# Performance work log

Hardware: AMD Instinct MI355X
Metric: run time of the kernel (lower is better)

The kernel has to match this reference:

```python
import jax, jax.numpy as jnp
import numpy as np

T = 2048; H = 1024; NH = 16; NKV = 4; HD = 64
E = 32; TOPK = 4; NG = 4; TG = 2; IM = 384; ISH = 384
ROT = HD // 2          # partial_rotary_factor = 0.5
EPS = 1e-5; RSF = 1.0; THETA = 10000.0


def setup_inputs() -> dict:
    ks = jax.random.split(jax.random.key(0), 12)
    g = lambda k, sh, sc=0.02: jax.random.normal(k, sh, jnp.float32) * sc
    return {
        "hidden_states": g(ks[0], (T, H), 1.0),
        "residual": g(ks[1], (T, H), 1.0),
        "in_ln_w": jnp.ones((H,), jnp.float32),
        "post_ln_w": jnp.ones((H,), jnp.float32),
        "q_norm_w": jnp.ones((HD,), jnp.float32),
        "k_norm_w": jnp.ones((HD,), jnp.float32),
        "Wqkv": g(ks[2], (H, (NH + 2 * NKV) * HD)),
        "Wo": g(ks[3], (NH * HD, H)),
        "Wg": g(ks[4], (H, E)),
        "gate_bias": g(ks[5], (E,), 0.1),
        "Wgu": g(ks[6], (E, H, 2 * IM)),
        "Wd": g(ks[7], (E, IM, H)),
        "Wgu_sh": g(ks[8], (H, 2 * ISH)),
        "Wd_sh": g(ks[9], (ISH, H)),
        "positions": jnp.arange(T, dtype=jnp.int32),
    }


def _rms(x, w):
    return x * jax.lax.rsqrt(jnp.mean(x * x, -1, keepdims=True) + EPS) * w


def _rope(x, pos):
    # neox-style rotary on the first ROT dims of each head; x: [T, nheads, HD]
    half = ROT // 2
    inv = THETA ** (-(jnp.arange(half, dtype=jnp.float32) * 2.0 / ROT))
    ang = pos.astype(jnp.float32)[:, None] * inv          # [T, half]
    c = jnp.cos(ang)[:, None, :]
    s = jnp.sin(ang)[:, None, :]
    x1, x2, rest = x[..., :half], x[..., half:ROT], x[..., ROT:]
    return jnp.concatenate([x1 * c - x2 * s, x1 * s + x2 * c, rest], -1)


def _layer(pos, hidden, residual, in_ln_w, post_ln_w, q_norm_w, k_norm_w,
           Wqkv, Wo, Wg, gate_bias, Wgu, Wd, Wgu_sh, Wd_sh):
    # fused add-RMSNorm (vllm RMSNorm(x, residual))
    residual = hidden + residual
    hidden = _rms(residual, in_ln_w)

    # self-attention (GQA, per-head qk-norm, partial rotary, causal)
    qkv = hidden @ Wqkv
    q = qkv[:, :NH * HD].reshape(T, NH, HD)
    k = qkv[:, NH * HD:(NH + NKV) * HD].reshape(T, NKV, HD)
    v = qkv[:, (NH + NKV) * HD:].reshape(T, NKV, HD)
    q = _rms(q, q_norm_w)
    k = _rms(k, k_norm_w)
    q = _rope(q, pos)
    k = _rope(k, pos)
    rep = NH // NKV
    k = jnp.repeat(k, rep, axis=1)
    v = jnp.repeat(v, rep, axis=1)
    scores = jnp.einsum('thd,shd->hts', q, k) * (HD ** -0.5)
    causal = pos[:, None] >= pos[None, :]
    scores = jnp.where(causal[None], scores, -jnp.inf)
    attn = jax.nn.softmax(scores, axis=-1)
    o = jnp.einsum('hts,shd->thd', attn, v).reshape(T, NH * HD)
    hidden = o @ Wo

    # post-attention fused add-RMSNorm
    residual = hidden + residual
    hidden = _rms(residual, post_ln_w)

    # --- Glm4MoE: grouped sigmoid top-k router with e_score_correction_bias ---
    logits = hidden.astype(jnp.float32) @ Wg            # gate runs in fp32
    scr = jax.nn.sigmoid(logits)                        # [T, E]
    sfc = scr + gate_bias                               # scores_for_choice
    # group score = sum of top-2 biased scores within each group
    gs = jnp.sum(jax.lax.top_k(sfc.reshape(T, NG, E // NG), 2)[0], -1)  # [T, NG]
    _, gidx = jax.lax.top_k(gs, TG)
    gmask = jnp.zeros((T, NG), jnp.float32).at[jnp.arange(T)[:, None], gidx].set(1.0)
    emask = jnp.repeat(gmask, E // NG, axis=1)          # [T, E]
    _, ids = jax.lax.top_k(jnp.where(emask > 0, sfc, -jnp.inf), TOPK)
    w = jnp.take_along_axis(scr, ids, axis=1)           # weights from unbiased scores
    w = w / jnp.sum(w, -1, keepdims=True)               # renormalize (norm_topk_prob)
    wdense = jnp.zeros((T, E), jnp.float32).at[jnp.arange(T)[:, None], ids].set(w)

    # routed experts: dense-over-experts reference for the grouped GEMM dispatch
    gu = jnp.einsum('th,ehi->tei', hidden, Wgu)         # [T, E, 2*IM]
    act = jax.nn.silu(gu[..., :IM]) * gu[..., IM:]      # SiluAndMul
    routed = jnp.einsum('te,tei,eih->th', wdense, act, Wd)

    # shared expert MLP
    gus = hidden @ Wgu_sh
    shared = (jax.nn.silu(gus[:, :ISH]) * gus[:, ISH:]) @ Wd_sh

    hidden = routed * RSF + shared
    return hidden, residual


def reference(hidden_states, residual, in_ln_w, post_ln_w, q_norm_w, k_norm_w,
              Wqkv, Wo, Wg, gate_bias, Wgu, Wd, Wgu_sh, Wd_sh, positions):
    return _layer(positions, hidden_states, residual, in_ln_w, post_ln_w,
                  q_norm_w, k_norm_w, Wqkv, Wo, Wg, gate_bias, Wgu, Wd,
                  Wgu_sh, Wd_sh)
```

## Files before the change

### kernel.cpp

```cpp
#include <hip/hip_runtime.h>
#include <math.h>

#define TT 2048
#define HH 1024
#define NHEADS 16
#define NKVH 4
#define HDIM 64
#define NEXP 32
#define TOPK_ 4
#define NGRP 4
#define IMID 384
#define ISHARED 384
#define QKV_W (24*64)
#define EPS_ 1e-5f
#define MAXSB 288
#define NSPLITS 80

typedef __attribute__((ext_vector_type(8))) short short8;
typedef __attribute__((ext_vector_type(4))) float f32x4;

__device__ __forceinline__ ushort f2bf(float x) {
  union { float f; unsigned u; } v; v.f = x;
  unsigned r = v.u + 0x7fffu + ((v.u >> 16) & 1u);
  return (ushort)(r >> 16);
}
__device__ __forceinline__ float bf2f(ushort u) {
  union { unsigned i; float f; } v; v.i = (unsigned)u << 16; return v.f;
}

__device__ __forceinline__ void gload16(const void* g, void* l) {
  __builtin_amdgcn_global_load_lds(
      (const __attribute__((address_space(1))) unsigned int*)g,
      (__attribute__((address_space(3))) unsigned int*)l, 16, 0, 0);
}

__device__ __forceinline__ short8 read_a_frag64(const ushort* As, int lg, int row) {
  return *(const short8*)(As + ((lg * 64 + (row ^ lg)) * 8));
}
__device__ __forceinline__ short8 read_b_frag(const ushort* Bs, int lg, int col) {
  int boff = (col * 16) ^ (((col >> 3) & 7) << 4);
  return *(const short8*)((const char*)Bs + lg * 1024 + boff);
}

__device__ __forceinline__ void stage_B_tile(const float* __restrict__ B, int ldb,
                                             int k0, int col0, ushort* Bs, int tid) {
  int a = tid >> 4;
  int cG = tid & 15;
  int k = 2 * a;
  const float* p0 = B + (size_t)(k0 + k) * ldb + col0 + cG * 4;
  const float* p1 = p0 + ldb;
  float4 r0 = *(const float4*)p0;
  float4 r1 = *(const float4*)p1;
  int gg = (k & 15) >> 2;
  int slot = (k & 3) + ((k >> 4) << 2);
  float v0[4] = {r0.x, r0.y, r0.z, r0.w};
  float v1[4] = {r1.x, r1.y, r1.z, r1.w};
  char* plane = (char*)Bs + gg * 1024;
  #pragma unroll
  for (int j = 0; j < 4; ++j) {
    int c = cG * 4 + j;
    unsigned pk = (unsigned)f2bf(v0[j]) | ((unsigned)f2bf(v1[j]) << 16);
    int boff = ((c * 16) ^ (((c >> 3) & 7) << 4)) + slot * 2;
    *(unsigned*)(plane + boff) = pk;
  }
}

__global__ __launch_bounds__(256) void pack_B_kernel(
    const float* __restrict__ src, ushort* __restrict__ dst, int N) {
  __shared__ ushort tileB[2048];
  int tid = threadIdx.x;
  stage_B_tile(src, N, blockIdx.y * 32, blockIdx.x * 64, tileB, tid);
  __syncthreads();
  size_t toff = ((size_t)blockIdx.y * gridDim.x + blockIdx.x) * 2048;
  *(short8*)(dst + toff + tid * 8) = *(const short8*)(tileB + tid * 8);
}

__global__ __launch_bounds__(256) void gemm64_bb(
    const ushort* __restrict__ Ab, const ushort* __restrict__ Bpk,
    float* __restrict__ C, int M, int N, int K) {
  __shared__ ushort As[4][2048];
  __shared__ ushort Bs[4][2048];
  int tid = threadIdx.x;
  int row0 = blockIdx.y * 64, col0 = blockIdx.x * 64;
  int ntn = N >> 6;
  int wid = tid >> 6, lane = tid & 63;
  int lg = lane >> 4, lr = lane & 15;
  int wrow = (wid >> 1) * 32, wcol = (wid & 1) * 32;
  const ushort* asrc = Ab + (size_t)(row0 + (lane ^ wid)) * K + wid * 8;
  const ushort* bsrc = Bpk + (size_t)blockIdx.x * 2048 + wid * 512 + lane * 8;
  const int NT = K >> 5;
  f32x4 acc[2][2] = {};

  auto issue = [&](int tt) {
    int b = tt & 3;
    gload16(asrc + tt * 32, &As[b][wid * 512]);
    gload16(bsrc + (size_t)tt * ntn * 2048, &Bs[b][wid * 512]);
  };
  issue(0); issue(1); issue(2);
  for (int t = 0; t < NT; ++t) {
    int ahead = NT - 1 - t;
    if (ahead >= 2)      asm volatile("s_waitcnt vmcnt(4)" ::: "memory");
    else if (ahead == 1) asm volatile("s_waitcnt vmcnt(2)" ::: "memory");
    else                 asm volatile("s_waitcnt vmcnt(0)" ::: "memory");
    __builtin_amdgcn_s_barrier();
    if (t + 3 < NT) issue(t + 3);
    int cb = t & 3;
    short8 af0 = read_a_frag64(&As[cb][0], lg, wrow + lr);
    short8 af1 = read_a_frag64(&As[cb][0], lg, wrow + 16 + lr);
    #pragma unroll
    for (int nn = 0; nn < 2; ++nn) {
      short8 bf_ = read_b_frag(&Bs[cb][0], lg, wcol + nn * 16 + lr);
      acc[0][nn] = __builtin_amdgcn_mfma_f32_16x16x32_bf16(af0, bf_, acc[0][nn], 0, 0, 0);
      acc[1][nn] = __builtin_amdgcn_mfma_f32_16x16x32_bf16(af1, bf_, acc[1][nn], 0, 0, 0);
    }
  }
  #pragma unroll
  for (int mm = 0; mm < 2; ++mm)
    #pragma unroll
    for (int nn = 0; nn < 2; ++nn) {
      int row = row0 + wrow + mm * 16 + lg * 4;
      int col = col0 + wcol + nn * 16 + lr;
      #pragma unroll
      for (int i = 0; i < 4; ++i)
        C[(size_t)(row + i) * N + col] = acc[mm][nn][i];
    }
}

__global__ __launch_bounds__(256) void moe_up_pk(
    const ushort* __restrict__ hln2b, const ushort* __restrict__ Wpk,
    const int* __restrict__ perm, const int* __restrict__ offs,
    const int* __restrict__ counts, const int* __restrict__ sb_e,
    const int* __restrict__ sb_base, const int* __restrict__ nsb,
    ushort* __restrict__ actb) {
  int b = blockIdx.x;
  int sb = ((b & 7) * 36) + (b >> 3);
  if (sb >= *nsb) return;
  int e = sb_e[sb];
  int base = sb_base[sb];
  int start = offs[e];
  int nt = min(32, counts[e] - base);
  int tid = threadIdx.x;
  int wid = tid >> 6, lane = tid & 63;
  int lg = lane >> 4, lr = lane & 15;
  int bz = blockIdx.y * 2 + (wid >> 1);
  int wcol = (wid & 1) * 32;
  int tok0 = perm[start + base + min(lr, nt - 1)] >> 2;
  int tok1 = perm[start + base + min(16 + lr, nt - 1)] >> 2;
  const ushort* a0p = hln2b + (size_t)tok0 * HH + lg * 8;
  const ushort* a1p = hln2b + (size_t)tok1 * HH + lg * 8;
  int c0 = wcol + lr, c1 = wcol + 16 + lr;
  int sw0 = (c0 * 16) ^ (((c0 >> 3) & 7) << 4);
  int sw1 = (c1 * 16) ^ (((c1 >> 3) & 7) << 4);
  const char* gbase = (const char*)Wpk + ((size_t)(e * 32) * 12 + bz) * 4096 + lg * 1024;
  const char* ubase = gbase + (size_t)6 * 4096;
  const size_t bstep = (size_t)12 * 4096;
  f32x4 accg[2][2] = {}, accu[2][2] = {};
  short8 a0c = *(const short8*)(a0p);
  short8 a1c = *(const short8*)(a1p);
  short8 g0c = *(const short8*)(gbase + sw0);
  short8 g1c = *(const short8*)(gbase + sw1);
  short8 u0c = *(const short8*)(ubase + sw0);
  short8 u1c = *(const short8*)(ubase + sw1);
  #pragma unroll 4
  for (int t = 0; t < 31; ++t) {
    const char* gb = gbase + (size_t)(t + 1) * bstep;
    const char* ub = ubase + (size_t)(t + 1) * bstep;
    short8 a0n = *(const short8*)(a0p + (t + 1) * 32);
    short8 a1n = *(const short8*)(a1p + (t + 1) * 32);
    short8 g0n = *(const short8*)(gb + sw0);
    short8 g1n = *(const short8*)(gb + sw1);
    short8 u0n = *(const short8*)(ub + sw0);
    short8 u1n = *(const short8*)(ub + sw1);
    accg[0][0] = __builtin_amdgcn_mfma_f32_16x16x32_bf16(a0c, g0c, accg[0][0], 0, 0, 0);
    accg[0][1] = __builtin_amdgcn_mfma_f32_16x16x32_bf16(a0c, g1c, accg[0][1], 0, 0, 0);
    accg[1][0] = __builtin_amdgcn_mfma_f32_16x16x32_bf16(a1c, g0c, accg[1][0], 0, 0, 0);
    accg[1][1] = __builtin_amdgcn_mfma_f32_16x16x32_bf16(a1c, g1c, accg[1][1], 0, 0, 0);
    accu[0][0] = __builtin_amdgcn_mfma_f32_16x16x32_bf16(a0c, u0c, accu[0][0], 0, 0, 0);
    accu[0][1] = __builtin_amdgcn_mfma_f32_16x16x32_bf16(a0c, u1c, accu[0][1], 0, 0, 0);
    accu[1][0] = __builtin_amdgcn_mfma_f32_16x16x32_bf16(a1c, u0c, accu[1][0], 0, 0, 0);
    accu[1][1] = __builtin_amdgcn_mfma_f32_16x16x32_bf16(a1c, u1c, accu[1][1], 0, 0, 0);
    a0c = a0n; a1c = a1n; g0c = g0n; g1c = g1n; u0c = u0n; u1c = u1n;
  }
  accg[0][0] = __builtin_amdgcn_mfma_f32_16x16x32_bf16(a0c, g0c, accg[0][0], 0, 0, 0);
  accg[0][1] = __builtin_amdgcn_mfma_f32_16x16x32_bf16(a0c, g1c, accg[0][1], 0, 0, 0);
  accg[1][0] = __builtin_amdgcn_mfma_f32_16x16x32_bf16(a1c, g0c, accg[1][0], 0, 0, 0);
  accg[1][1] = __builtin_amdgcn_mfma_f32_16x16x32_bf16(a1c, g1c, accg[1][1], 0, 0, 0);
  accu[0][0] = __builtin_amdgcn_mfma_f32_16x16x32_bf16(a0c, u0c, accu[0][0], 0, 0, 0);
  accu[0][1] = __builtin_amdgcn_mfma_f32_16x16x32_bf16(a0c, u1c, accu[0][1], 0, 0, 0);
  accu[1][0] = __builtin_amdgcn_mfma_f32_16x16x32_bf16(a1c, u0c, accu[1][0], 0, 0, 0);
  accu[1][1] = __builtin_amdgcn_mfma_f32_16x16x32_bf16(a1c, u1c, accu[1][1], 0, 0, 0);
  #pragma unroll
  for (int mm = 0; mm < 2; ++mm)
    #pragma unroll
    for (int nn = 0; nn < 2; ++nn) {
      int pcol = bz * 64 + wcol + ((lr >> 2) << 3) + (nn << 2) + (lr & 3);
      #pragma unroll
      for (int i = 0; i < 4; ++i) {
        int rr = mm * 16 + lg * 4 + i;
        if (rr < nt) {
          float gv = accg[mm][nn][i], uv = accu[mm][nn][i];
          float av = gv / (1.f + expf(-gv)) * uv;
          actb[(size_t)(start + base + rr) * IMID + pcol] = f2bf(av);
        }
      }
    }
}

__global__ __launch_bounds__(256) void moe_down_pk(
    const ushort* __restrict__ actb, const ushort* __restrict__ Wpk,
    const int* __restrict__ offs, const int* __restrict__ counts,
    const int* __restrict__ sb_e, const int* __restrict__ sb_base,
    const int* __restrict__ nsb, ushort* __restrict__ partialb) {
  int b = blockIdx.x;
  int sb = ((b & 7) * 36) + (b >> 3);
  if (sb >= *nsb) return;
  int e = sb_e[sb];
  int base = sb_base[sb];
  int start = offs[e];
  int nt = min(32, counts[e] - base);
  int tid = threadIdx.x;
  int wid = tid >> 6, lane = tid & 63;
  int lg = lane >> 4, lr = lane & 15;
  int nct = blockIdx.y * 2 + (wid >> 1);
  int wcol = (wid & 1) * 32;
  const ushort* a0p = actb + (size_t)(start + base + min(lr, nt - 1)) * IMID + lg * 8;
  const ushort* a1p = actb + (size_t)(start + base + min(16 + lr, nt - 1)) * IMID + lg * 8;
  int c0 = wcol + lr, c1 = wcol + 16 + lr;
  int sw0 = (c0 * 16) ^ (((c0 >> 3) & 7) << 4);
  int sw1 = (c1 * 16) ^ (((c1 >> 3) & 7) << 4);
  const char* bbase = (const char*)Wpk + ((size_t)(e * 12) * 16 + nct) * 4096 + lg * 1024;
  const size_t bstep = (size_t)16 * 4096;
  f32x4 acc[2][2] = {};
  short8 a0c = *(const short8*)(a0p);
  short8 a1c = *(const short8*)(a1p);
  short8 b0c = *(const short8*)(bbase + sw0);
  short8 b1c = *(const short8*)(bbase + sw1);
  #pragma unroll 4
  for (int t = 0; t < 11; ++t) {
    const char* bb = bbase + (size_t)(t + 1) * bstep;
    short8 a0n = *(const short8*)(a0p + (t + 1) * 32);
    short8 a1n = *(const short8*)(a1p + (t + 1) * 32);
    short8 b0n = *(const short8*)(bb + sw0);
    short8 b1n = *(const short8*)(bb + sw1);
    acc[0][0] = __builtin_amdgcn_mfma_f32_16x16x32_bf16(a0c, b0c, acc[0][0], 0, 0, 0);
    acc[0][1] = __builtin_amdgcn_mfma_f32_16x16x32_bf16(a0c, b1c, acc[0][1], 0, 0, 0);
    acc[1][0] = __builtin_amdgcn_mfma_f32_16x16x32_bf16(a1c, b0c, acc[1][0], 0, 0, 0);
    acc[1][1] = __builtin_amdgcn_mfma_f32_16x16x32_bf16(a1c, b1c, acc[1][1], 0, 0, 0);
    a0c = a0n; a1c = a1n; b0c = b0n; b1c = b1n;
  }
  acc[0][0] = __builtin_amdgcn_mfma_f32_16x16x32_bf16(a0c, b0c, acc[0][0], 0, 0, 0);
  acc[0][1] = __builtin_amdgcn_mfma_f32_16x16x32_bf16(a0c, b1c, acc[0][1], 0, 0, 0);
  acc[1][0] = __builtin_amdgcn_mfma_f32_16x16x32_bf16(a1c, b0c, acc[1][0], 0, 0, 0);
  acc[1][1] = __builtin_amdgcn_mfma_f32_16x16x32_bf16(a1c, b1c, acc[1][1], 0, 0, 0);
  #pragma unroll
  for (int mm = 0; mm < 2; ++mm)
    #pragma unroll
    for (int nn = 0; nn < 2; ++nn)
      #pragma unroll
      for (int i = 0; i < 4; ++i) {
        int rr = mm * 16 + lg * 4 + i;
        if (rr < nt)
          partialb[(size_t)(start + base + rr) * HH + nct * 64 + wcol + nn * 16 + lr] = f2bf(acc[mm][nn][i]);
      }
}

__global__ __launch_bounds__(256) void add_rms_kernel(
    const float* __restrict__ a, const float* __restrict__ b,
    const float* __restrict__ w, float* __restrict__ sum_out,
    float* __restrict__ ln_out, ushort* __restrict__ lnb) {
  int t = blockIdx.x, tid = threadIdx.x;
  float4 x = reinterpret_cast<const float4*>(a + (size_t)t*HH)[tid];
  float4 y = reinterpret_cast<const float4*>(b + (size_t)t*HH)[tid];
  x.x += y.x; x.y += y.y; x.z += y.z; x.w += y.w;
  float ss = x.x*x.x + x.y*x.y + x.z*x.z + x.w*x.w;
  #pragma unroll
  for (int off = 1; off < 64; off <<= 1) ss += __shfl_xor(ss, off);
  __shared__ float wsum[4];
  int wid = tid >> 6, lane = tid & 63;
  if (lane == 0) wsum[wid] = ss;
  __syncthreads();
  float tot = wsum[0] + wsum[1] + wsum[2] + wsum[3];
  float r = rsqrtf(tot * (1.0f/HH) + EPS_);
  reinterpret_cast<float4*>(sum_out + (size_t)t*HH)[tid] = x;
  float4 wl = reinterpret_cast<const float4*>(w)[tid];
  float4 o = make_float4(x.x*r*wl.x, x.y*r*wl.y, x.z*r*wl.z, x.w*r*wl.w);
  reinterpret_cast<float4*>(ln_out + (size_t)t*HH)[tid] = o;
  ushort4 ub;
  ub.x = f2bf(o.x); ub.y = f2bf(o.y); ub.z = f2bf(o.z); ub.w = f2bf(o.w);
  int dst = ((tid >> 3) << 5) + ((tid & 3) << 3) + (((tid >> 2) & 1) << 2);
  *(ushort4*)(lnb + (size_t)t * HH + dst) = ub;
}

__global__ __launch_bounds__(256) void qk_norm_rope_kernel(
    float* __restrict__ qkv, const float* __restrict__ qw,
    const float* __restrict__ kw, const int* __restrict__ pos) {
  int t = blockIdx.x;
  int hh = blockIdx.y * 4 + (threadIdx.x >> 6);
  int lane = threadIdx.x & 63;
  float* p = qkv + (size_t)t * QKV_W + hh * HDIM;
  float x = p[lane];
  float ss = x * x;
  #pragma unroll
  for (int off = 1; off < 64; off <<= 1) ss += __shfl_xor(ss, off);
  float r = rsqrtf(ss * (1.0f/HDIM) + EPS_);
  float wv = (hh < NHEADS ? qw : kw)[lane];
  float xn = x * r * wv;
  float partner = __shfl_xor(xn, 16);
  float out = xn;
  if (lane < 32) {
    int i = lane & 15;
    float inv = powf(10000.0f, -(float)i / 16.0f);
    float ang = (float)pos[t] * inv;
    float cv = cosf(ang), sv = sinf(ang);
    out = (lane < 16) ? (xn * cv - partner * sv) : (partner * sv + xn * cv);
  }
  p[lane] = out;
}

__global__ __launch_bounds__(256) void pack_KV_kernel(
    const float* __restrict__ qkv, ushort* __restrict__ Kpk,
    ushort* __restrict__ Vpk) {
  __shared__ ushort kimg[2048];
  __shared__ ushort vimg[2048];
  int tid = threadIdx.x;
  int kt = blockIdx.x, kvh = blockIdx.y;
  {
    int c = tid >> 7, t2 = tid & 127;
    int g = t2 & 3, r = t2 >> 2;
    const float* kp = qkv + (size_t)(kt*32 + r) * QKV_W + NHEADS*HDIM + kvh*HDIM + 32*c + 4*g;
    float4 h0 = *(const float4*)kp;
    float4 h1 = *(const float4*)(kp + 16);
    short8 v;
    v[0]=(short)f2bf(h0.x); v[1]=(short)f2bf(h0.y); v[2]=(short)f2bf(h0.z); v[3]=(short)f2bf(h0.w);
    v[4]=(short)f2bf(h1.x); v[5]=(short)f2bf(h1.y); v[6]=(short)f2bf(h1.z); v[7]=(short)f2bf(h1.w);
    *(short8*)(kimg + c*1024 + (g*32 + (r^g))*8) = v;
  }
  stage_B_tile(qkv + (size_t)(NHEADS+NKVH)*HDIM + (size_t)kvh*HDIM, QKV_W, kt*32, 0, vimg, tid);
  __syncthreads();
  size_t toff = ((size_t)(kvh * (TT/32) + kt)) * 2048;
  *(short8*)(Kpk + toff + tid * 8) = *(const short8*)(kimg + tid * 8);
  *(short8*)(Vpk + toff + tid * 8) = *(const short8*)(vimg + tid * 8);
}

__global__ __launch_bounds__(256) void attn_v3_kernel(
    const float* __restrict__ qkv, const ushort* __restrict__ Kpk,
    const ushort* __restrict__ Vpk, ushort* __restrict__ ob,
    float* __restrict__ po, float* __restrict__ pl) {
  __shared__ ushort Ks[3][2048];
  __shared__ ushort Vs[3][2048];
  int tid = threadIdx.x;
  int wid = tid >> 6, lane = tid & 63;
  int lg = lane >> 4, lr = lane & 15;
  int h = blockIdx.y;
  int f = blockIdx.x;
  int g = 0;
  while (f >= 4 * (g + 1) * (g + 2)) ++g;
  int r_ = f - 4 * g * (g + 1);
  int ns = g + 1;
  int qb = 8 * g + r_ / ns;
  int s = r_ % ns;
  int tiles_total = 2 * qb + 2;
  int per = (tiles_total + ns - 1) / ns;
  int lo = s * per;
  int nloc = min(per, tiles_total - lo);
  int kvh = h >> 2;
  int q0 = qb * 64 + wid * 16;
  int qg = q0 + lr;
  const float SCL = 0.125f * 1.44269504f;
  const float FM = 16.0f;

  const float* qrow = qkv + (size_t)qg * QKV_W + h * HDIM;
  short8 qfr[2];
  #pragma unroll
  for (int c = 0; c < 2; ++c) {
    float4 a = *(const float4*)(qrow + 32*c + 4*lg);
    float4 b = *(const float4*)(qrow + 32*c + 4*lg + 16);
    short8 v;
    v[0]=(short)f2bf(a.x*SCL); v[1]=(short)f2bf(a.y*SCL); v[2]=(short)f2bf(a.z*SCL); v[3]=(short)f2bf(a.w*SCL);
    v[4]=(short)f2bf(b.x*SCL); v[5]=(short)f2bf(b.y*SCL); v[6]=(short)f2bf(b.z*SCL); v[7]=(short)f2bf(b.w*SCL);
    qfr[c] = v;
  }

  const ushort* ksrc = Kpk + (size_t)(kvh * (TT/32) + lo) * 2048 + wid * 512 + lane * 8;
  const ushort* vsrc = Vpk + (size_t)(kvh * (TT/32) + lo) * 2048 + wid * 512 + lane * 8;

  f32x4 o_acc[4] = {};
  float l_st = 0.f;

  auto issue = [&](int tt) {
    int b = tt % 3;
    gload16(ksrc + (size_t)tt * 2048, &Ks[b][wid * 512]);
    gload16(vsrc + (size_t)tt * 2048, &Vs[b][wid * 512]);
  };
  issue(0);
  if (nloc > 1) issue(1);
  for (int tt = 0; tt < nloc; ++tt) {
    if (tt < nloc - 1) asm volatile("s_waitcnt vmcnt(2)" ::: "memory");
    else               asm volatile("s_waitcnt vmcnt(0)" ::: "memory");
    __builtin_amdgcn_s_barrier();
    if (tt + 2 < nloc) issue(tt + 2);
    int t = lo + tt;
    if (t * 32 > q0 + 15) continue;
    int cb = tt % 3;
    f32x4 st[2];
    #pragma unroll
    for (int n = 0; n < 2; ++n) {
      short8 kf0 = *(const short8*)(&Ks[cb][(lg*32 + ((16*n + lr) ^ lg)) * 8]);
      short8 kf1 = *(const short8*)(&Ks[cb][1024 + (lg*32 + ((16*n + lr) ^ lg)) * 8]);
      f32x4 z = {};
      z = __builtin_amdgcn_mfma_f32_16x16x32_bf16(kf0, qfr[0], z, 0, 0, 0);
      st[n] = __builtin_amdgcn_mfma_f32_16x16x32_bf16(kf1, qfr[1], z, 0, 0, 0);
    }
    float p[2][4];
    float psum = 0.f;
    if (t * 32 + 31 <= q0) {
      #pragma unroll
      for (int n = 0; n < 2; ++n)
        #pragma unroll
        for (int i = 0; i < 4; ++i) {
          float pv = exp2f(st[n][i] - FM);
          p[n][i] = pv; psum += pv;
        }
    } else {
      #pragma unroll
      for (int n = 0; n < 2; ++n)
        #pragma unroll
        for (int i = 0; i < 4; ++i) {
          int kvg = t*32 + 16*n + 4*lg + i;
          float pv = (kvg <= qg) ? exp2f(st[n][i] - FM) : 0.f;
          p[n][i] = pv; psum += pv;
        }
    }
    psum += __shfl_xor(psum, 16);
    psum += __shfl_xor(psum, 32);
    l_st += psum;
    union { unsigned u[4]; short8 s8; } pu;
    asm volatile("v_cvt_pk_bf16_f32 %0, %1, %2" : "=v"(pu.u[0]) : "v"(p[0][0]), "v"(p[0][1]));
    asm volatile("v_cvt_pk_bf16_f32 %0, %1, %2" : "=v"(pu.u[1]) : "v"(p[0][2]), "v"(p[0][3]));
    asm volatile("v_cvt_pk_bf16_f32 %0, %1, %2" : "=v"(pu.u[2]) : "v"(p[1][0]), "v"(p[1][1]));
    asm volatile("v_cvt_pk_bf16_f32 %0, %1, %2" : "=v"(pu.u[3]) : "v"(p[1][2]), "v"(p[1][3]));
    short8 pa = pu.s8;
    #pragma unroll
    for (int nd = 0; nd < 4; ++nd) {
      short8 vf = read_b_frag(&Vs[cb][0], lg, 16*nd + lr);
      o_acc[nd] = __builtin_amdgcn_mfma_f32_16x16x32_bf16(pa, vf, o_acc[nd], 0, 0, 0);
    }
  }

  if (ns == 1) {
    #pragma unroll
    for (int i = 0; i < 4; ++i) {
      float lrow = __shfl(l_st, 4*lg + i);
      float inv = 1.0f / lrow;
      int row = q0 + 4*lg + i;
      ushort* op = ob + (size_t)row * (NHEADS*HDIM) + h * HDIM;
      #pragma unroll
      for (int nd = 0; nd < 4; ++nd) {
        int pcol = ((nd >> 1) << 5) + ((lr >> 2) << 3) + ((nd & 1) << 2) + (lr & 3);
        op[pcol] = f2bf(o_acc[nd][i] * inv);
      }
    }
  } else {
    float* pob = po + ((size_t)f * NHEADS + h) * 4096;
    #pragma unroll
    for (int nd = 0; nd < 4; ++nd)
      #pragma unroll
      for (int i = 0; i < 4; ++i)
        pob[(wid * 16 + lg * 4 + i) * 64 + 16 * nd + lr] = o_acc[nd][i];
    if (lg == 0)
      pl[((size_t)f * NHEADS + h) * 64 + wid * 16 + lr] = l_st;
  }
}

__global__ __launch_bounds__(256) void attn_combine_kernel(
    const float* __restrict__ po, const float* __restrict__ pl,
    ushort* __restrict__ ob) {
  int h = blockIdx.x;
  int qb = 8 + blockIdx.y;
  int g = qb >> 3;
  int ns = g + 1;
  int f0 = 4 * g * (g + 1) + (qb - 8 * g) * ns;
  int tid = threadIdx.x;
  int r = tid >> 2, c = tid & 3;
  float acc[16] = {};
  float lsum = 0.f;
  for (int s = 0; s < ns; ++s) {
    size_t base = ((size_t)(f0 + s) * NHEADS + h) * 4096 + r * 64 + c * 16;
    #pragma unroll
    for (int j = 0; j < 4; ++j) {
      float4 v = *(const float4*)(po + base + j * 4);
      acc[j*4+0] += v.x; acc[j*4+1] += v.y; acc[j*4+2] += v.z; acc[j*4+3] += v.w;
    }
    lsum += pl[((size_t)(f0 + s) * NHEADS + h) * 64 + r];
  }
  float inv = 1.0f / lsum;
  int row = qb * 64 + r;
  ushort* op = ob + (size_t)row * (NHEADS*HDIM) + h * HDIM + (c >> 1) * 32 + (c & 1) * 4;
  #pragma unroll
  for (int a = 0; a < 4; ++a) {
    ushort4 u;
    u.x = f2bf(acc[a*4+0] * inv); u.y = f2bf(acc[a*4+1] * inv);
    u.z = f2bf(acc[a*4+2] * inv); u.w = f2bf(acc[a*4+3] * inv);
    *(ushort4*)(op + a * 8) = u;
  }
}

__global__ __launch_bounds__(256) void router_kernel(
    const float* __restrict__ hln, const float* __restrict__ Wg,
    const float* __restrict__ bias, int* __restrict__ sel_e,
    float* __restrict__ sel_w) {
  __shared__ float hid[4][HH];
  int tid = threadIdx.x, wid = tid >> 6, lane = tid & 63;
  int t = blockIdx.x * 4 + wid;
  const float4* src = (const float4*)(hln + (size_t)t * HH);
  float4* dst = (float4*)hid[wid];
  #pragma unroll
  for (int j = 0; j < 4; ++j) dst[j * 64 + lane] = src[j * 64 + lane];
  int e = lane & 31, half = lane >> 5;
  const float* wp = Wg + (size_t)(half * 512) * NEXP + e;
  const float* hp = hid[wid] + half * 512;
  float p = 0.f;
  #pragma unroll 8
  for (int h = 0; h < 512; ++h) p += hp[h] * wp[(size_t)h * NEXP];
  p += __shfl_xor(p, 32);
  float sc = 1.0f / (1.0f + expf(-p));
  float sfc = sc + bias[e];
  float m1 = sfc, m2 = -1e30f;
  #pragma unroll
  for (int off = 1; off <= 4; off <<= 1) {
    float om1 = __shfl_xor(m1, off), om2 = __shfl_xor(m2, off);
    float hi_ = fmaxf(m1, om1);
    float lo_ = fmaxf(fminf(m1, om1), fmaxf(m2, om2));
    m1 = hi_; m2 = lo_;
  }
  float gs = m1 + m2;
  float gv[4] = {__shfl(gs, 0), __shfl(gs, 8), __shfl(gs, 16), __shfl(gs, 24)};
  int g1 = 0; float b1 = gv[0];
  #pragma unroll
  for (int g = 1; g < 4; ++g) if (gv[g] > b1) { b1 = gv[g]; g1 = g; }
  int g2 = -1; float b2 = -1e30f;
  #pragma unroll
  for (int g = 0; g < 4; ++g) if (g != g1 && gv[g] > b2) { b2 = gv[g]; g2 = g; }
  bool keep = ((e >> 3) == g1) || ((e >> 3) == g2);
  float cand = keep ? sfc : -1e30f;
  int ids[4]; float wv[4]; float wsum = 0.f;
  #pragma unroll
  for (int s = 0; s < 4; ++s) {
    float v = cand; int ix = e;
    #pragma unroll
    for (int off = 1; off < 64; off <<= 1) {
      float ov = __shfl_xor(v, off); int oix = __shfl_xor(ix, off);
      if (ov > v || (ov == v && oix < ix)) { v = ov; ix = oix; }
    }
    ids[s] = ix;
    if (e == ix) cand = -1e30f;
    float w = __shfl(sc, ix);
    wv[s] = w; wsum += w;
  }
  if (lane == 0) {
    #pragma unroll
    for (int s = 0; s < 4; ++s) {
      sel_e[t * 4 + s] = ids[s];
      sel_w[t * 4 + s] = wv[s] / wsum;
    }
  }
}

__global__ __launch_bounds__(256) void count_kernel(
    const int* __restrict__ sel_e, int* __restrict__ counts) {
  int e = blockIdx.x, tid = threadIdx.x;
  int c = 0;
  for (int i = tid; i < TT * TOPK_; i += 256) c += (sel_e[i] == e);
  #pragma unroll
  for (int off = 1; off < 64; off <<= 1) c += __shfl_xor(c, off);
  __shared__ int wsum[4];
  if ((tid & 63) == 0) wsum[tid >> 6] = c;
  __syncthreads();
  if (tid == 0) counts[e] = wsum[0] + wsum[1] + wsum[2] + wsum[3];
}

__global__ void scan_kernel(const int* __restrict__ counts,
                            int* __restrict__ offs, int* __restrict__ cursor,
                            int* __restrict__ sb_e, int* __restrict__ sb_base,
                            int* __restrict__ nsb) {
  if (threadIdx.x == 0) {
    int acc = 0, n = 0;
    for (int e = 0; e < NEXP; ++e) {
      offs[e] = acc; cursor[e] = acc;
      int c = counts[e];
      for (int b = 0; b < c; b += 32) { sb_e[n] = e; sb_base[n] = b; ++n; }
      acc += c;
    }
    *nsb = n;
  }
}

__global__ void scatter_kernel(const int* __restrict__ sel_e,
                               int* __restrict__ cursor, int* __restrict__ perm,
                               int* __restrict__ ipos) {
  int i = blockIdx.x * 256 + threadIdx.x;
  if (i < TT * TOPK_) {
    int e = sel_e[i];
    int pos = atomicAdd(&cursor[e], 1);
    perm[pos] = i;
    ipos[i] = pos;
  }
}

__global__ __launch_bounds__(256) void silu_shared_kernel(
    const float* __restrict__ gus, ushort* __restrict__ shsb) {
  int i = blockIdx.x * 256 + threadIdx.x;
  if (i < TT * (ISHARED/4)) {
    int t = i / (ISHARED/4), k = i % (ISHARED/4);
    const float* gp = gus + (size_t)t * (2*ISHARED) + k * 4;
    float4 g4 = *(const float4*)gp;
    float4 u4 = *(const float4*)(gp + ISHARED);
    ushort4 r;
    r.x = f2bf(g4.x / (1.f + expf(-g4.x)) * u4.x);
    r.y = f2bf(g4.y / (1.f + expf(-g4.y)) * u4.y);
    r.z = f2bf(g4.z / (1.f + expf(-g4.z)) * u4.z);
    r.w = f2bf(g4.w / (1.f + expf(-g4.w)) * u4.w);
    int pdst = ((k >> 3) << 5) + ((k & 3) << 3) + (((k >> 2) & 1) << 2);
    *(ushort4*)(shsb + (size_t)t * ISHARED + pdst) = r;
  }
}

__global__ __launch_bounds__(256) void final_combine_kernel(
    const ushort* __restrict__ partialb, const float* __restrict__ sel_w,
    const int* __restrict__ ipos, const float* __restrict__ shared_out,
    float* __restrict__ out_hidden) {
  int t = blockIdx.x, tid = threadIdx.x;
  float w0 = sel_w[t*4], w1 = sel_w[t*4+1], w2 = sel_w[t*4+2], w3 = sel_w[t*4+3];
  int p0 = ipos[t*4], p1 = ipos[t*4+1], p2 = ipos[t*4+2], p3 = ipos[t*4+3];
  ushort4 a0 = *(const ushort4*)(partialb + (size_t)p0*HH + tid*4);
  ushort4 a1 = *(const ushort4*)(partialb + (size_t)p1*HH + tid*4);
  ushort4 a2 = *(const ushort4*)(partialb + (size_t)p2*HH + tid*4);
  ushort4 a3 = *(const ushort4*)(partialb + (size_t)p3*HH + tid*4);
  float4 sh = reinterpret_cast<const float4*>(shared_out + (size_t)t*HH)[tid];
  float4 r;
  r.x = (w0*bf2f(a0.x) + w1*bf2f(a1.x) + w2*bf2f(a2.x) + w3*bf2f(a3.x)) + sh.x;
  r.y = (w0*bf2f(a0.y) + w1*bf2f(a1.y) + w2*bf2f(a2.y) + w3*bf2f(a3.y)) + sh.y;
  r.z = (w0*bf2f(a0.z) + w1*bf2f(a1.z) + w2*bf2f(a2.z) + w3*bf2f(a3.z)) + sh.z;
  r.w = (w0*bf2f(a0.w) + w1*bf2f(a1.w) + w2*bf2f(a2.w) + w3*bf2f(a3.w)) + sh.w;
  reinterpret_cast<float4*>(out_hidden + (size_t)t*HH)[tid] = r;
}

extern "C" void kernel_launch(void* const* d_in, const int* in_sizes, int n_in,
                              void* d_out, int out_size, void* d_ws, size_t ws_size,
                              hipStream_t stream) {
  const float* hidden   = (const float*)d_in[0];
  const float* residual = (const float*)d_in[1];
  const float* in_ln_w  = (const float*)d_in[2];
  const float* post_ln_w= (const float*)d_in[3];
  const float* q_norm_w = (const float*)d_in[4];
  const float* k_norm_w = (const float*)d_in[5];
  const float* Wqkv     = (const float*)d_in[6];
  const float* Wo       = (const float*)d_in[7];
  const float* Wg       = (const float*)d_in[8];
  const float* gate_bias= (const float*)d_in[9];
  const float* Wgu      = (const float*)d_in[10];
  const float* Wd       = (const float*)d_in[11];
  const float* Wgu_sh   = (const float*)d_in[12];
  const float* Wd_sh    = (const float*)d_in[13];
  const int*   positions= (const int*)d_in[14];
  float* out = (float*)d_out;

  float* f = (float*)d_ws;
  size_t off = 0;
  float* R_A   = f + off; off += (size_t)TT*HH;
  float* HLN   = f + off; off += (size_t)TT*HH;
  float* QKV   = f + off; off += (size_t)TT*QKV_W;
  float* OATT  = f + off; off += (size_t)TT*HH;
  float* HLN2  = f + off; off += (size_t)TT*HH;
  float* SELW  = f + off; off += (size_t)TT*TOPK_;
  float* PO    = f + off; off += (size_t)NSPLITS*NHEADS*4096;
  float* PL    = f + off; off += (size_t)NSPLITS*NHEADS*64;
  ushort* HLNB  = (ushort*)(f + off); off += (size_t)TT*HH/2;
  ushort* HLN2B = (ushort*)(f + off); off += (size_t)TT*HH/2;
  ushort* OATTB = (ushort*)(f + off); off += (size_t)TT*HH/2;
  ushort* SHSB  = (ushort*)(f + off); off += (size_t)TT*ISHARED/2;
  ushort* KPK   = (ushort*)(f + off); off += (size_t)NKVH*(TT/32)*2048/2;
  ushort* VPK   = (ushort*)(f + off); off += (size_t)NKVH*(TT/32)*2048/2;
  ushort* ACTB  = (ushort*)(f + off); off += (size_t)(TT*TOPK_ + 128)*IMID/2;
  ushort* PARTB = (ushort*)(f + off); off += (size_t)TT*TOPK_*HH/2;
  ushort* PK_QKV = (ushort*)(f + off); off += (size_t)HH*QKV_W/2;
  ushort* PK_WO  = (ushort*)(f + off); off += (size_t)HH*HH/2;
  ushort* PK_WGU = (ushort*)(f + off); off += (size_t)NEXP*HH*(2*IMID)/2;
  ushort* PK_WD  = (ushort*)(f + off); off += (size_t)NEXP*IMID*HH/2;
  ushort* PK_GUSH= (ushort*)(f + off); off += (size_t)HH*(2*ISHARED)/2;
  ushort* PK_DSH = (ushort*)(f + off); off += (size_t)ISHARED*HH/2;
  int* ibase   = (int*)(f + off);
  int* SELE    = ibase;
  int* PERM    = ibase + TT*TOPK_;
  int* IPOS    = ibase + 2*TT*TOPK_;
  int* COUNTS  = ibase + 3*TT*TOPK_;
  int* OFFS    = COUNTS + NEXP;
  int* CURSOR  = OFFS + NEXP;
  int* SB_E    = CURSOR + NEXP;
  int* SB_BASE = SB_E + MAXSB;
  int* NSB     = SB_BASE + MAXSB;

  pack_B_kernel<<<dim3(QKV_W/64, HH/32), 256, 0, stream>>>(Wqkv, PK_QKV, QKV_W);
  pack_B_kernel<<<dim3(HH/64, HH/32), 256, 0, stream>>>(Wo, PK_WO, HH);
  pack_B_kernel<<<dim3((2*IMID)/64, NEXP*HH/32), 256, 0, stream>>>(Wgu, PK_WGU, 2*IMID);
  pack_B_kernel<<<dim3(HH/64, NEXP*IMID/32), 256, 0, stream>>>(Wd, PK_WD, HH);
  pack_B_kernel<<<dim3((2*ISHARED)/64, HH/32), 256, 0, stream>>>(Wgu_sh, PK_GUSH, 2*ISHARED);
  pack_B_kernel<<<dim3(HH/64, ISHARED/32), 256, 0, stream>>>(Wd_sh, PK_DSH, HH);

  add_rms_kernel<<<TT, 256, 0, stream>>>(hidden, residual, in_ln_w, R_A, HLN, HLNB);
  gemm64_bb<<<dim3(QKV_W/64, TT/64), 256, 0, stream>>>(HLNB, PK_QKV, QKV, TT, QKV_W, HH);
  qk_norm_rope_kernel<<<dim3(TT, 5), 256, 0, stream>>>(QKV, q_norm_w, k_norm_w, positions);
  pack_KV_kernel<<<dim3(TT/32, NKVH), 256, 0, stream>>>(QKV, KPK, VPK);
  attn_v3_kernel<<<dim3(NSPLITS, NHEADS), 256, 0, stream>>>(QKV, KPK, VPK, OATTB, PO, PL);
  attn_combine_kernel<<<dim3(NHEADS, 24), 256, 0, stream>>>(PO, PL, OATTB);
  gemm64_bb<<<dim3(HH/64, TT/64), 256, 0, stream>>>(OATTB, PK_WO, HLN, TT, HH, HH);
  add_rms_kernel<<<TT, 256, 0, stream>>>(HLN, R_A, post_ln_w, out + (size_t)TT*HH, HLN2, HLN2B);
  router_kernel<<<TT/4, 256, 0, stream>>>(HLN2, Wg, gate_bias, SELE, SELW);
  count_kernel<<<NEXP, 256, 0, stream>>>(SELE, COUNTS);
  scan_kernel<<<1, 64, 0, stream>>>(COUNTS, OFFS, CURSOR, SB_E, SB_BASE, NSB);
  scatter_kernel<<<(TT*TOPK_ + 255)/256, 256, 0, stream>>>(SELE, CURSOR, PERM, IPOS);
  moe_up_pk<<<dim3(MAXSB, 3), 256, 0, stream>>>(HLN2B, PK_WGU, PERM, OFFS, COUNTS, SB_E, SB_BASE, NSB, ACTB);
  moe_down_pk<<<dim3(MAXSB, 8), 256, 0, stream>>>(ACTB, PK_WD, OFFS, COUNTS, SB_E, SB_BASE, NSB, PARTB);
  gemm64_bb<<<dim3((2*ISHARED)/64, TT/64), 256, 0, stream>>>(HLN2B, PK_GUSH, QKV, TT, 2*ISHARED, HH);
  silu_shared_kernel<<<(TT*(ISHARED/4) + 255)/256, 256, 0, stream>>>(QKV, SHSB);
  gemm64_bb<<<dim3(HH/64, TT/64), 256, 0, stream>>>(SHSB, PK_DSH, OATT, TT, HH, ISHARED);
  final_combine_kernel<<<TT, 256, 0, stream>>>(PARTB, SELW, IPOS, OATT, out);
}
```

Measured before the change: 361.6 us.

## Repartition MoE up-projection warps by row and batch weight packing tiles per block

```diff
diff --git a/kernel.cpp b/kernel.cpp
--- a/kernel.cpp
+++ b/kernel.cpp
@@ -65,14 +65,20 @@
   }
 }
 
-__global__ __launch_bounds__(256) void pack_B_kernel(
+__global__ __launch_bounds__(256) void pack_B4_kernel(
     const float* __restrict__ src, ushort* __restrict__ dst, int N) {
   __shared__ ushort tileB[2048];
   int tid = threadIdx.x;
-  stage_B_tile(src, N, blockIdx.y * 32, blockIdx.x * 64, tileB, tid);
-  __syncthreads();
-  size_t toff = ((size_t)blockIdx.y * gridDim.x + blockIdx.x) * 2048;
-  *(short8*)(dst + toff + tid * 8) = *(const short8*)(tileB + tid * 8);
+  int ntn = gridDim.x;
+  #pragma unroll
+  for (int kk = 0; kk < 4; ++kk) {
+    int kt = blockIdx.y * 4 + kk;
+    stage_B_tile(src, N, kt * 32, blockIdx.x * 64, tileB, tid);
+    __syncthreads();
+    size_t toff = ((size_t)kt * ntn + blockIdx.x) * 2048;
+    *(short8*)(dst + toff + tid * 8) = *(const short8*)(tileB + tid * 8);
+    __syncthreads();
+  }
 }
 
 __global__ __launch_bounds__(256) void gemm64_bb(
@@ -142,21 +148,21 @@
   int tid = threadIdx.x;
   int wid = tid >> 6, lane = tid & 63;
   int lg = lane >> 4, lr = lane & 15;
-  int bz = blockIdx.y * 2 + (wid >> 1);
+  int bz = blockIdx.y;
+  int rh = wid >> 1;
   int wcol = (wid & 1) * 32;
-  int tok0 = perm[start + base + min(lr, nt - 1)] >> 2;
-  int tok1 = perm[start + base + min(16 + lr, nt - 1)] >> 2;
-  const ushort* a0p = hln2b + (size_t)tok0 * HH + lg * 8;
-  const ushort* a1p = hln2b + (size_t)tok1 * HH + lg * 8;
+  int row = rh * 16 + lr;
+  int rowc = min(row, nt - 1);
+  int tok = perm[start + base + rowc] >> 2;
+  const ushort* ap = hln2b + (size_t)tok * HH + lg * 8;
   int c0 = wcol + lr, c1 = wcol + 16 + lr;
   int sw0 = (c0 * 16) ^ (((c0 >> 3) & 7) << 4);
   int sw1 = (c1 * 16) ^ (((c1 >> 3) & 7) << 4);
   const char* gbase = (const char*)Wpk + ((size_t)(e * 32) * 12 + bz) * 4096 + lg * 1024;
   const char* ubase = gbase + (size_t)6 * 4096;
   const size_t bstep = (size_t)12 * 4096;
-  f32x4 accg[2][2] = {}, accu[2][2] = {};
-  short8 a0c = *(const short8*)(a0p);
-  short8 a1c = *(const short8*)(a1p);
+  f32x4 ag0 = {}, ag1 = {}, au0 = {}, au1 = {};
+  short8 ac  = *(const short8*)ap;
   short8 g0c = *(const short8*)(gbase + sw0);
   short8 g1c = *(const short8*)(gbase + sw1);
   short8 u0c = *(const short8*)(ubase + sw0);
@@ -165,45 +171,35 @@
   for (int t = 0; t < 31; ++t) {
     const char* gb = gbase + (size_t)(t + 1) * bstep;
     const char* ub = ubase + (size_t)(t + 1) * bstep;
-    short8 a0n = *(const short8*)(a0p + (t + 1) * 32);
-    short8 a1n = *(const short8*)(a1p + (t + 1) * 32);
+    short8 an  = *(const short8*)(ap + (t + 1) * 32);
     short8 g0n = *(const short8*)(gb + sw0);
     short8 g1n = *(const short8*)(gb + sw1);
     short8 u0n = *(const short8*)(ub + sw0);
     short8 u1n = *(const short8*)(ub + sw1);
-    accg[0][0] = __builtin_amdgcn_mfma_f32_16x16x32_bf16(a0c, g0c, accg[0][0], 0, 0, 0);
-    accg[0][1] = __builtin_amdgcn_mfma_f32_16x16x32_bf16(a0c, g1c, accg[0][1], 0, 0, 0);
-    accg[1][0] = __builtin_amdgcn_mfma_f32_16x16x32_bf16(a1c, g0c, accg[1][0], 0, 0, 0);
-    accg[1][1] = __builtin_amdgcn_mfma_f32_16x16x32_bf16(a1c, g1c, accg[1][1], 0, 0, 0);
-    accu[0][0] = __builtin_amdgcn_mfma_f32_16x16x32_bf16(a0c, u0c, accu[0][0], 0, 0, 0);
-    accu[0][1] = __builtin_amdgcn_mfma_f32_16x16x32_bf16(a0c, u1c, accu[0][1], 0, 0, 0);
-    accu[1][0] = __builtin_amdgcn_mfma_f32_16x16x32_bf16(a1c, u0c, accu[1][0], 0, 0, 0);
-    accu[1][1] = __builtin_amdgcn_mfma_f32_16x16x32_bf16(a1c, u1c, accu[1][1], 0, 0, 0);
-    a0c = a0n; a1c = a1n; g0c = g0n; g1c = g1n; u0c = u0n; u1c = u1n;
-  }
-  accg[0][0] = __builtin_amdgcn_mfma_f32_16x16x32_bf16(a0c, g0c, accg[0][0], 0, 0, 0);
-  accg[0][1] = __builtin_amdgcn_mfma_f32_16x16x32_bf16(a0c, g1c, accg[0][1], 0, 0, 0);
-  accg[1][0] = __builtin_amdgcn_mfma_f32_16x16x32_bf16(a1c, g0c, accg[1][0], 0, 0, 0);
-  accg[1][1] = __builtin_amdgcn_mfma_f32_16x16x32_bf16(a1c, g1c, accg[1][1], 0, 0, 0);
-  accu[0][0] = __builtin_amdgcn_mfma_f32_16x16x32_bf16(a0c, u0c, accu[0][0], 0, 0, 0);
-  accu[0][1] = __builtin_amdgcn_mfma_f32_16x16x32_bf16(a0c, u1c, accu[0][1], 0, 0, 0);
-  accu[1][0] = __builtin_amdgcn_mfma_f32_16x16x32_bf16(a1c, u0c, accu[1][0], 0, 0, 0);
-  accu[1][1] = __builtin_amdgcn_mfma_f32_16x16x32_bf16(a1c, u1c, accu[1][1], 0, 0, 0);
-  #pragma unroll
-  for (int mm = 0; mm < 2; ++mm)
-    #pragma unroll
-    for (int nn = 0; nn < 2; ++nn) {
-      int pcol = bz * 64 + wcol + ((lr >> 2) << 3) + (nn << 2) + (lr & 3);
-      #pragma unroll
-      for (int i = 0; i < 4; ++i) {
-        int rr = mm * 16 + lg * 4 + i;
-        if (rr < nt) {
-          float gv = accg[mm][nn][i], uv = accu[mm][nn][i];
-          float av = gv / (1.f + expf(-gv)) * uv;
-          actb[(size_t)(start + base + rr) * IMID + pcol] = f2bf(av);
-        }
+    ag0 = __builtin_amdgcn_mfma_f32_16x16x32_bf16(ac, g0c, ag0, 0, 0, 0);
+    ag1 = __builtin_amdgcn_mfma_f32_16x16x32_bf16(ac, g1c, ag1, 0, 0, 0);
+    au0 = __builtin_amdgcn_mfma_f32_16x16x32_bf16(ac, u0c, au0, 0, 0, 0);
+    au1 = __builtin_amdgcn_mfma_f32_16x16x32_bf16(ac, u1c, au1, 0, 0, 0);
+    ac = an; g0c = g0n; g1c = g1n; u0c = u0n; u1c = u1n;
+  }
+  ag0 = __builtin_amdgcn_mfma_f32_16x16x32_bf16(ac, g0c, ag0, 0, 0, 0);
+  ag1 = __builtin_amdgcn_mfma_f32_16x16x32_bf16(ac, g1c, ag1, 0, 0, 0);
+  au0 = __builtin_amdgcn_mfma_f32_16x16x32_bf16(ac, u0c, au0, 0, 0, 0);
+  au1 = __builtin_amdgcn_mfma_f32_16x16x32_bf16(ac, u1c, au1, 0, 0, 0);
+  f32x4 ag[2] = {ag0, ag1}, au[2] = {au0, au1};
+  #pragma unroll
+  for (int nn = 0; nn < 2; ++nn) {
+    int pcol = bz * 64 + wcol + ((lr >> 2) << 3) + (nn << 2) + (lr & 3);
+    #pragma unroll
+    for (int i = 0; i < 4; ++i) {
+      int rr = rh * 16 + lg * 4 + i;
+      if (rr < nt) {
+        float gv = ag[nn][i], uv = au[nn][i];
+        float av = gv / (1.f + expf(-gv)) * uv;
+        actb[(size_t)(start + base + rr) * IMID + pcol] = f2bf(av);
       }
     }
+  }
 }
 
 __global__ __launch_bounds__(256) void moe_down_pk(
@@ -700,12 +696,12 @@
   int* SB_BASE = SB_E + MAXSB;
   int* NSB     = SB_BASE + MAXSB;
 
-  pack_B_kernel<<<dim3(QKV_W/64, HH/32), 256, 0, stream>>>(Wqkv, PK_QKV, QKV_W);
-  pack_B_kernel<<<dim3(HH/64, HH/32), 256, 0, stream>>>(Wo, PK_WO, HH);
-  pack_B_kernel<<<dim3((2*IMID)/64, NEXP*HH/32), 256, 0, stream>>>(Wgu, PK_WGU, 2*IMID);
-  pack_B_kernel<<<dim3(HH/64, NEXP*IMID/32), 256, 0, stream>>>(Wd, PK_WD, HH);
-  pack_B_kernel<<<dim3((2*ISHARED)/64, HH/32), 256, 0, stream>>>(Wgu_sh, PK_GUSH, 2*ISHARED);
-  pack_B_kernel<<<dim3(HH/64, ISHARED/32), 256, 0, stream>>>(Wd_sh, PK_DSH, HH);
+  pack_B4_kernel<<<dim3(QKV_W/64, HH/32/4), 256, 0, stream>>>(Wqkv, PK_QKV, QKV_W);
+  pack_B4_kernel<<<dim3(HH/64, HH/32/4), 256, 0, stream>>>(Wo, PK_WO, HH);
+  pack_B4_kernel<<<dim3((2*IMID)/64, NEXP*HH/32/4), 256, 0, stream>>>(Wgu, PK_WGU, 2*IMID);
+  pack_B4_kernel<<<dim3(HH/64, NEXP*IMID/32/4), 256, 0, stream>>>(Wd, PK_WD, HH);
+  pack_B4_kernel<<<dim3((2*ISHARED)/64, HH/32/4), 256, 0, stream>>>(Wgu_sh, PK_GUSH, 2*ISHARED);
+  pack_B4_kernel<<<dim3(HH/64, ISHARED/32/4), 256, 0, stream>>>(Wd_sh, PK_DSH, HH);
 
   add_rms_kernel<<<TT, 256, 0, stream>>>(hidden, residual, in_ln_w, R_A, HLN, HLNB);
   gemm64_bb<<<dim3(QKV_W/64, TT/64), 256, 0, stream>>>(HLNB, PK_QKV, QKV, TT, QKV_W, HH);
@@ -719,7 +715,7 @@
   count_kernel<<<NEXP, 256, 0, stream>>>(SELE, COUNTS);
   scan_kernel<<<1, 64, 0, stream>>>(COUNTS, OFFS, CURSOR, SB_E, SB_BASE, NSB);
   scatter_kernel<<<(TT*TOPK_ + 255)/256, 256, 0, stream>>>(SELE, CURSOR, PERM, IPOS);
-  moe_up_pk<<<dim3(MAXSB, 3), 256, 0, stream>>>(HLN2B, PK_WGU, PERM, OFFS, COUNTS, SB_E, SB_BASE, NSB, ACTB);
+  moe_up_pk<<<dim3(MAXSB, 6), 256, 0, stream>>>(HLN2B, PK_WGU, PERM, OFFS, COUNTS, SB_E, SB_BASE, NSB, ACTB);
   moe_down_pk<<<dim3(MAXSB, 8), 256, 0, stream>>>(ACTB, PK_WD, OFFS, COUNTS, SB_E, SB_BASE, NSB, PARTB);
   gemm64_bb<<<dim3((2*ISHARED)/64, TT/64), 256, 0, stream>>>(HLN2B, PK_GUSH, QKV, TT, 2*ISHARED, HH);
   silu_shared_kernel<<<(TT*(ISHARED/4) + 255)/256, 256, 0, stream>>>(QKV, SHSB);
```

Result: slower. 379.9 us (+5.1%).

## Restage MoE down-proj through triple-buffered LDS with async global_load_lds

Applied to the files above, without the earlier changes.

```diff
diff --git a/kernel.cpp b/kernel.cpp
--- a/kernel.cpp
+++ b/kernel.cpp
@@ -34,6 +34,9 @@
       (__attribute__((address_space(3))) unsigned int*)l, 16, 0, 0);
 }
 
+__device__ __forceinline__ short8 read_a_frag32(const ushort* As, int lg, int row) {
+  return *(const short8*)(As + ((lg * 32 + (row ^ lg)) * 8));
+}
 __device__ __forceinline__ short8 read_a_frag64(const ushort* As, int lg, int row) {
   return *(const short8*)(As + ((lg * 64 + (row ^ lg)) * 8));
 }
@@ -218,50 +221,50 @@
   int base = sb_base[sb];
   int start = offs[e];
   int nt = min(32, counts[e] - base);
+  __shared__ ushort As[3][1024];
+  __shared__ ushort Bs[3][2048];
   int tid = threadIdx.x;
+  int bz = blockIdx.y, col0 = bz * 64;
   int wid = tid >> 6, lane = tid & 63;
   int lg = lane >> 4, lr = lane & 15;
-  int nct = blockIdx.y * 2 + (wid >> 1);
-  int wcol = (wid & 1) * 32;
-  const ushort* a0p = actb + (size_t)(start + base + min(lr, nt - 1)) * IMID + lg * 8;
-  const ushort* a1p = actb + (size_t)(start + base + min(16 + lr, nt - 1)) * IMID + lg * 8;
-  int c0 = wcol + lr, c1 = wcol + 16 + lr;
-  int sw0 = (c0 * 16) ^ (((c0 >> 3) & 7) << 4);
-  int sw1 = (c1 * 16) ^ (((c1 >> 3) & 7) << 4);
-  const char* bbase = (const char*)Wpk + ((size_t)(e * 12) * 16 + nct) * 4096 + lg * 1024;
-  const size_t bstep = (size_t)16 * 4096;
-  f32x4 acc[2][2] = {};
-  short8 a0c = *(const short8*)(a0p);
-  short8 a1c = *(const short8*)(a1p);
-  short8 b0c = *(const short8*)(bbase + sw0);
-  short8 b1c = *(const short8*)(bbase + sw1);
-  #pragma unroll 4
-  for (int t = 0; t < 11; ++t) {
-    const char* bb = bbase + (size_t)(t + 1) * bstep;
-    short8 a0n = *(const short8*)(a0p + (t + 1) * 32);
-    short8 a1n = *(const short8*)(a1p + (t + 1) * 32);
-    short8 b0n = *(const short8*)(bb + sw0);
-    short8 b1n = *(const short8*)(bb + sw1);
-    acc[0][0] = __builtin_amdgcn_mfma_f32_16x16x32_bf16(a0c, b0c, acc[0][0], 0, 0, 0);
-    acc[0][1] = __builtin_amdgcn_mfma_f32_16x16x32_bf16(a0c, b1c, acc[0][1], 0, 0, 0);
-    acc[1][0] = __builtin_amdgcn_mfma_f32_16x16x32_bf16(a1c, b0c, acc[1][0], 0, 0, 0);
-    acc[1][1] = __builtin_amdgcn_mfma_f32_16x16x32_bf16(a1c, b1c, acc[1][1], 0, 0, 0);
-    a0c = a0n; a1c = a1n; b0c = b0n; b1c = b1n;
-  }
-  acc[0][0] = __builtin_amdgcn_mfma_f32_16x16x32_bf16(a0c, b0c, acc[0][0], 0, 0, 0);
-  acc[0][1] = __builtin_amdgcn_mfma_f32_16x16x32_bf16(a0c, b1c, acc[0][1], 0, 0, 0);
-  acc[1][0] = __builtin_amdgcn_mfma_f32_16x16x32_bf16(a1c, b0c, acc[1][0], 0, 0, 0);
-  acc[1][1] = __builtin_amdgcn_mfma_f32_16x16x32_bf16(a1c, b1c, acc[1][1], 0, 0, 0);
-  #pragma unroll
-  for (int mm = 0; mm < 2; ++mm)
-    #pragma unroll
-    for (int nn = 0; nn < 2; ++nn)
-      #pragma unroll
-      for (int i = 0; i < 4; ++i) {
-        int rr = mm * 16 + lg * 4 + i;
-        if (rr < nt)
-          partialb[(size_t)(start + base + rr) * HH + nct * 64 + wcol + nn * 16 + lr] = f2bf(acc[mm][nn][i]);
-      }
+  int wrow = (wid >> 1) * 16, wcol = (wid & 1) * 32;
+  const ushort* bt0 = Wpk + ((size_t)(e * 12) * 16 + bz) * 2048 + wid * 512 + lane * 8;
+  int ga = wid * 2 + (lane >> 5);
+  const ushort* asrcA = actb + (size_t)(start + base + ((lane & 31) ^ ga)) * IMID + ga * 8;
+  const int NT = IMID >> 5;
+  f32x4 acc[2] = {};
+
+  auto issue = [&](int tt) {
+    int bb = tt % 3;
+    if (wid < 2) gload16(asrcA + tt * 32, &As[bb][wid * 512]);
+    gload16(bt0 + (size_t)tt * 16 * 2048, &Bs[bb][wid * 512]);
+  };
+  issue(0); issue(1);
+  for (int t = 0; t < NT; ++t) {
+    if (t < NT - 1) {
+      if (wid < 2) asm volatile("s_waitcnt vmcnt(2)" ::: "memory");
+      else         asm volatile("s_waitcnt vmcnt(1)" ::: "memory");
+    } else {
+      asm volatile("s_waitcnt vmcnt(0)" ::: "memory");
+    }
+    __builtin_amdgcn_s_barrier();
+    if (t + 2 < NT) issue(t + 2);
+    int cb = t % 3;
+    short8 af = read_a_frag32(&As[cb][0], lg, wrow + lr);
+    #pragma unroll
+    for (int nn = 0; nn < 2; ++nn) {
+      short8 bf_ = read_b_frag(&Bs[cb][0], lg, wcol + nn * 16 + lr);
+      acc[nn] = __builtin_amdgcn_mfma_f32_16x16x32_bf16(af, bf_, acc[nn], 0, 0, 0);
+    }
+  }
+  #pragma unroll
+  for (int nn = 0; nn < 2; ++nn)
+    #pragma unroll
+    for (int i = 0; i < 4; ++i) {
+      int rr = wrow + lg * 4 + i;
+      if (rr < nt)
+        partialb[(size_t)(start + base + rr) * HH + col0 + wcol + nn * 16 + lr] = f2bf(acc[nn][i]);
+    }
 }
 
 __global__ __launch_bounds__(256) void add_rms_kernel(
@@ -720,7 +723,7 @@
   scan_kernel<<<1, 64, 0, stream>>>(COUNTS, OFFS, CURSOR, SB_E, SB_BASE, NSB);
   scatter_kernel<<<(TT*TOPK_ + 255)/256, 256, 0, stream>>>(SELE, CURSOR, PERM, IPOS);
   moe_up_pk<<<dim3(MAXSB, 3), 256, 0, stream>>>(HLN2B, PK_WGU, PERM, OFFS, COUNTS, SB_E, SB_BASE, NSB, ACTB);
-  moe_down_pk<<<dim3(MAXSB, 8), 256, 0, stream>>>(ACTB, PK_WD, OFFS, COUNTS, SB_E, SB_BASE, NSB, PARTB);
+  moe_down_pk<<<dim3(MAXSB, HH/64), 256, 0, stream>>>(ACTB, PK_WD, OFFS, COUNTS, SB_E, SB_BASE, NSB, PARTB);
   gemm64_bb<<<dim3((2*ISHARED)/64, TT/64), 256, 0, stream>>>(HLN2B, PK_GUSH, QKV, TT, 2*ISHARED, HH);
   silu_shared_kernel<<<(TT*(ISHARED/4) + 255)/256, 256, 0, stream>>>(QKV, SHSB);
   gemm64_bb<<<dim3(HH/64, TT/64), 256, 0, stream>>>(SHSB, PK_DSH, OATT, TT, HH, ISHARED);
```

Result: faster. 341.9 us (-5.4%).
